# Optimization experiments

Measured on AMD Instinct MI355X. Metric: run time of the kernel, lower is better.

The kernel has to match this reference:

```python
import jax, jax.numpy as jnp
import numpy as np

DIM = 1024


def setup_inputs() -> dict:
    key = jax.random.key(0)
    ks = jax.random.split(key, 9)
    s = 1.0 / np.sqrt(DIM)
    x = jax.random.normal(ks[0], (4, 4096, DIM), dtype=jnp.float32)
    Wq = jax.random.uniform(ks[1], (DIM, DIM), jnp.float32, -s, s)
    bq = jax.random.uniform(ks[2], (DIM,), jnp.float32, -s, s)
    Wk = jax.random.uniform(ks[3], (DIM, DIM), jnp.float32, -s, s)
    bk = jax.random.uniform(ks[4], (DIM,), jnp.float32, -s, s)
    Wv = jax.random.uniform(ks[5], (DIM, DIM), jnp.float32, -s, s)
    bv = jax.random.uniform(ks[6], (DIM,), jnp.float32, -s, s)
    Wo = jax.random.uniform(ks[7], (DIM, DIM), jnp.float32, -s, s)
    bo = jax.random.uniform(ks[8], (DIM,), jnp.float32, -s, s)
    return {"x": x, "Wq": Wq, "bq": bq, "Wk": Wk, "bk": bk,
            "Wv": Wv, "bv": bv, "Wo": Wo, "bo": bo}


def reference(x, Wq, bq, Wk, bk, Wv, bv, Wo, bo):
    # x: [B, N, C]; weights stored as [C, C] (torch Linear applies x @ W.T,
    # here we store W already transposed so x @ W matches).
    scale = x.shape[-1] ** (-0.5)
    q = x @ Wq + bq                                  # [B, N, C]
    k = x @ Wk + bk
    v = x @ Wv + bv
    scores = jnp.einsum('bnc,bmc->bnm', q, k) * scale  # [B, N, N]
    attn = jax.nn.softmax(scores, axis=-1)
    out = jnp.einsum('bnm,bmc->bnc', attn, v)          # [B, N, C]
    return out @ Wo + bo
```

## Files before the change

### kernel.cpp

```cpp
#include <hip/hip_runtime.h>
#include <hip/hip_bf16.h>
#include <stdint.h>

typedef __bf16 bf16_8 __attribute__((ext_vector_type(8)));
typedef float  f32x4  __attribute__((ext_vector_type(4)));

#define GLL(g, l) __builtin_amdgcn_global_load_lds(                         \
    (__attribute__((address_space(1))) void*)(g),                           \
    (__attribute__((address_space(3))) void*)(l), 16, 0, 0)

__global__ void sniff_dtype(const uint32_t* __restrict__ x, uint32_t* __restrict__ flag)
{
    uint32_t w = x[threadIdx.x];
    uint32_t e = (w >> 23) & 0xFF;
    int isf32 = (e >= 100 && e <= 145) ? 1 : 0;
    unsigned long long m = __ballot(isf32);
    if (threadIdx.x == 0) *flag = (__popcll(m) >= 48) ? 1u : 0u;
}

__global__ __launch_bounds__(256)
void convert_to_bf16(const void* __restrict__ in, long elemOff,
                     __bf16* __restrict__ out, long n, const uint32_t* __restrict__ flag)
{
    long i = ((long)blockIdx.x * 256 + threadIdx.x) * 8;
    if (i >= n) return;
    bf16_8 o;
    if (*flag) {
        const float* p = (const float*)in + elemOff + i;
        float4 a = *(const float4*)p;
        float4 b = *(const float4*)(p + 4);
        o[0]=(__bf16)a.x; o[1]=(__bf16)a.y; o[2]=(__bf16)a.z; o[3]=(__bf16)a.w;
        o[4]=(__bf16)b.x; o[5]=(__bf16)b.y; o[6]=(__bf16)b.z; o[7]=(__bf16)b.w;
    } else {
        o = *(const bf16_8*)((const __bf16*)in + elemOff + i);
    }
    *(bf16_8*)(out + i) = o;
}

__global__ __launch_bounds__(256)
void convert_bias4(const void* b0, const void* b1, const void* b2, const void* b3,
                   __bf16* o0, __bf16* o1, __bf16* o2, __bf16* o3,
                   const uint32_t* __restrict__ flag)
{
    const void* in = (blockIdx.x == 0) ? b0 : (blockIdx.x == 1) ? b1
                   : (blockIdx.x == 2) ? b2 : b3;
    __bf16* out = (blockIdx.x == 0) ? o0 : (blockIdx.x == 1) ? o1
                : (blockIdx.x == 2) ? o2 : o3;
    long i = (long)threadIdx.x * 8;
    if (i >= 1024) return;
    bf16_8 o;
    if (*flag) {
        const float* p = (const float*)in + i;
        float4 a = *(const float4*)p;
        float4 b = *(const float4*)(p + 4);
        o[0]=(__bf16)a.x; o[1]=(__bf16)a.y; o[2]=(__bf16)a.z; o[3]=(__bf16)a.w;
        o[4]=(__bf16)b.x; o[5]=(__bf16)b.y; o[6]=(__bf16)b.z; o[7]=(__bf16)b.w;
    } else {
        o = *(const bf16_8*)((const __bf16*)in + i);
    }
    *(bf16_8*)(out + i) = o;
}

__global__ __launch_bounds__(256)
void convT_w4(const void* W0, const void* W1, const void* W2, const void* W3,
              __bf16* T0, __bf16* T1, __bf16* T2, __bf16* T3,
              const uint32_t* __restrict__ flag)
{
    const void* W = (blockIdx.z == 0) ? W0 : (blockIdx.z == 1) ? W1
                  : (blockIdx.z == 2) ? W2 : W3;
    __bf16* WT    = (blockIdx.z == 0) ? T0 : (blockIdx.z == 1) ? T1
                  : (blockIdx.z == 2) ? T2 : T3;
    __shared__ __bf16 tile[64][72];
    const int bc = blockIdx.x * 64, br = blockIdx.y * 64;
    const int c = threadIdx.x & 63, r0 = threadIdx.x >> 6;
    const bool f32 = (*flag != 0);
#pragma unroll
    for (int i = 0; i < 16; i++) {
        int r = i * 4 + r0;
        long idx = (long)(br + r) * 1024 + bc + c;
        float v = f32 ? ((const float*)W)[idx] : (float)((const __bf16*)W)[idx];
        tile[r][c] = (__bf16)v;
    }
    __syncthreads();
#pragma unroll
    for (int i = 0; i < 16; i++) {
        int r = i * 4 + r0;
        WT[(long)(bc + r) * 1024 + br + c] = tile[c][r];
    }
}

template<int BM_T, int BN_T, int GX, int GY, int GZ, int RX, int RY,
         int OUT_MODE, bool HAS_BIAS>
__global__ __launch_bounds__(512, 2)
void gemm_big(const __bf16* __restrict__ A, int lda,
              const __bf16* __restrict__ BT, int ldb,
              void* __restrict__ C, int ldc,
              const __bf16* __restrict__ bias,
              int kLen, long zCbytes, float scale,
              float* __restrict__ rowSums)
{
    constexpr int MT  = BM_T / 32;
    constexpr int NT  = BN_T / 64;
    constexpr int AG  = BM_T / 128;
    constexpr int BG  = BN_T / 128;
    constexpr int NLD = 2 * (AG + BG);

    constexpr int NRX = GX / RX;
    static_assert(NRX * ((GY * GZ) / RY) == 8, "regions must cover 8 XCDs");
    static_assert(RX * RY == (GX * GY * GZ) / 8, "region size = blocks/XCD");

    __shared__ __align__(16) __bf16 As[2][2 * BM_T * 32];
    __shared__ __align__(16) __bf16 Bs[2][2 * BN_T * 32];

    const int t    = threadIdx.x;
    const int wave = t >> 6;
    const int lane = t & 63;
    const int quad = lane >> 4;
    const int lrow = lane & 15;
    const int wm   = wave >> 2;
    const int wn   = wave & 3;

    const int h   = (int)blockIdx.x;
    const int xcd = h & 7;
    const int s   = h >> 3;
    const int bx  = (xcd % NRX) * RX + (s % RX);
    const int byz = (xcd / NRX) * RY + (s / RX);
    const int by  = byz % GY;
    const int bz  = byz / GY;

    const long m0  = (long)by * BM_T;
    const long n0  = (long)bx * BN_T;

    A  += (long)bz * kLen;
    BT += (long)bz * kLen;
    C   = (void*)((char*)C + (long)bz * zCbytes);

    const int sr = lane >> 2;
    const int sc = (lane & 3) ^ ((lane >> 3) & 3);
    const int sl = (lrow >> 1) & 3;

    const __bf16* aSrc = A + (m0 + wave * (BM_T / 8) + sr) * (long)lda + sc * 8;
    const __bf16* bSrc = BT + (n0 + wave * (BN_T / 8) + sr) * (long)ldb + sc * 8;

    f32x4 zero4 = {0.f, 0.f, 0.f, 0.f};
    f32x4 acc[MT][NT];
#pragma unroll
    for (int mt = 0; mt < MT; mt++)
#pragma unroll
        for (int nt = 0; nt < NT; nt++) acc[mt][nt] = zero4;

    auto STAGE = [&](int buf, const __bf16* aS, const __bf16* bS) {
        __bf16* aD = &As[buf][0] + wave * (BM_T / 8) * 32;
        __bf16* bD = &Bs[buf][0] + wave * (BN_T / 8) * 32;
#pragma unroll
        for (int kk = 0; kk < 2; kk++) {
#pragma unroll
            for (int g = 0; g < AG; g++)
                GLL(aS + kk * 32 + (long)g * 16 * lda,
                    aD + kk * (BM_T * 32) + g * 512);
#pragma unroll
            for (int g = 0; g < BG; g++)
                GLL(bS + kk * 32 + (long)g * 16 * ldb,
                    bD + kk * (BN_T * 32) + g * 512);
        }
    };

    auto COMPUTE = [&](int buf) {
#pragma unroll
        for (int kk = 0; kk < 2; kk++) {
            bf16_8 af[MT], bfr[NT];
#pragma unroll
            for (int mt = 0; mt < MT; mt++)
                af[mt] = *(const bf16_8*)(&As[buf][0] + kk * (BM_T * 32)
                           + (wm * (BM_T / 2) + mt * 16 + lrow) * 32 + (quad ^ sl) * 8);
#pragma unroll
            for (int nt = 0; nt < NT; nt++)
                bfr[nt] = *(const bf16_8*)(&Bs[buf][0] + kk * (BN_T * 32)
                           + (wn * (BN_T / 4) + nt * 16 + lrow) * 32 + (quad ^ sl) * 8);

#pragma unroll
            for (int mt = 0; mt < MT; mt++)
#pragma unroll
                for (int nt = 0; nt < NT; nt++)
                    acc[mt][nt] = __builtin_amdgcn_mfma_f32_16x16x32_bf16(
                                      af[mt], bfr[nt], acc[mt][nt], 0, 0, 0);
        }
    };

    STAGE(0, aSrc, bSrc);
    aSrc += 64; bSrc += 64;

    int cur = 0;
    for (int k0 = 64; k0 < kLen; k0 += 64) {
        STAGE(cur ^ 1, aSrc, bSrc);
        aSrc += 64; bSrc += 64;
        if constexpr (NLD == 8) asm volatile("s_waitcnt vmcnt(8)" ::: "memory");
        else                    asm volatile("s_waitcnt vmcnt(6)" ::: "memory");
        __builtin_amdgcn_s_barrier();
        __builtin_amdgcn_sched_barrier(0);
        __builtin_amdgcn_s_setprio(1);
        COMPUTE(cur);
        __builtin_amdgcn_s_setprio(0);
        asm volatile("s_waitcnt lgkmcnt(0)" ::: "memory");
        __builtin_amdgcn_s_barrier();
        __builtin_amdgcn_sched_barrier(0);
        cur ^= 1;
    }
    asm volatile("s_waitcnt vmcnt(0)" ::: "memory");
    __builtin_amdgcn_s_barrier();
    __builtin_amdgcn_sched_barrier(0);
    __builtin_amdgcn_s_setprio(1);
    COMPUTE(cur);
    __builtin_amdgcn_s_setprio(0);

    if (OUT_MODE == 3) {
#pragma unroll
        for (int mt = 0; mt < MT; mt++) {
#pragma unroll
            for (int i = 0; i < 4; i++) {
                long row = m0 + wm * (BM_T / 2) + mt * 16 + quad * 4 + i;
                float rs = 0.f;
#pragma unroll
                for (int nt = 0; nt < NT; nt++) {
                    long col = n0 + wn * (BN_T / 4) + nt * 16 + lrow;
                    float e = exp2f(acc[mt][nt][i] * scale);
                    ((__bf16*)C)[row * (long)ldc + col] = (__bf16)e;
                    rs += e;
                }
                rs += __shfl_xor(rs, 1);
                rs += __shfl_xor(rs, 2);
                rs += __shfl_xor(rs, 4);
                rs += __shfl_xor(rs, 8);
                if (lrow == 0) atomicAdd(&rowSums[row], rs);
            }
        }
        return;
    }

#pragma unroll
    for (int mt = 0; mt < MT; mt++) {
#pragma unroll
        for (int nt = 0; nt < NT; nt++) {
#pragma unroll
            for (int i = 0; i < 4; i++) {
                long row = m0 + wm * (BM_T / 2) + mt * 16 + quad * 4 + i;
                long col = n0 + wn * (BN_T / 4) + nt * 16 + lrow;
                float v = acc[mt][nt][i] * scale;
                if (HAS_BIAS) v += (float)bias[col];
                if (OUT_MODE == 0)      ((__bf16*)C)[row * (long)ldc + col] = (__bf16)v;
                else if (OUT_MODE == 1) ((__bf16*)C)[col * (long)ldc + row] = (__bf16)v;
                else                    ((float* )C)[row * (long)ldc + col] = v;
            }
        }
    }
}

template<int BN_T, int OUT_MODE, bool HAS_BIAS>
__global__ __launch_bounds__(256)
void gemm_bt(const __bf16* __restrict__ A, int lda,
             const __bf16* __restrict__ BT, int ldb,
             void* __restrict__ C, int ldc,
             const __bf16* __restrict__ bias,
             int M, int N, int kLen, long zCbytes, float scale,
             float* __restrict__ rowSums)
{
    constexpr int NT    = (BN_T == 128) ? 4 : 2;
    constexpr int BHALF = BN_T * 32;
    __shared__ __align__(16) __bf16 As[2][2 * 128 * 32];
    __shared__ __align__(16) __bf16 Bs[2][2 * BHALF];

    const int t    = threadIdx.x;
    const int wave = t >> 6;
    const int lane = t & 63;
    const int quad = lane >> 4;
    const int lrow = lane & 15;
    const int wm   = wave >> 1;
    const int wn   = wave & 1;
    const long m0  = (long)blockIdx.y * 128;
    const long n0  = (long)blockIdx.x * BN_T;

    A  += (long)blockIdx.z * kLen;
    BT += (long)blockIdx.z * kLen;
    C   = (void*)((char*)C + (long)blockIdx.z * zCbytes);

    const int sr = lane >> 2;
    const int sc = (lane & 3) ^ ((lane >> 3) & 3);

    const __bf16* aSrc = A + (m0 + wave * 32 + sr) * (long)lda + sc * 8;
    const __bf16* bSrc = (BN_T == 128)
        ? BT + (n0 + wave * 32 + sr) * (long)ldb + sc * 8
        : BT + (n0 + wave * 16 + sr) * (long)ldb + sc * 8;
    const long a16 = 16L * lda, b16 = 16L * ldb;

    f32x4 zero4 = {0.f, 0.f, 0.f, 0.f};
    f32x4 acc[4][NT];
#pragma unroll
    for (int mt = 0; mt < 4; mt++)
#pragma unroll
        for (int nt = 0; nt < NT; nt++) acc[mt][nt] = zero4;

    const int sl = (lrow >> 1) & 3;

    auto STAGE = [&](int buf, const __bf16* aS, const __bf16* bS) {
        __bf16* aD = &As[buf][0] + wave * 1024;
        __bf16* bD = &Bs[buf][0] + wave * (BN_T == 128 ? 1024 : 512);
        GLL(aS, aD);
        GLL(aS + a16, aD + 512);
        GLL(bS, bD);
        if (BN_T == 128) GLL(bS + b16, bD + 512);
        GLL(aS + 32, aD + 4096);
        GLL(aS + a16 + 32, aD + 4096 + 512);
        GLL(bS + 32, bD + BHALF);
        if (BN_T == 128) GLL(bS + b16 + 32, bD + BHALF + 512);
    };

    auto COMPUTE = [&](int buf) {
#pragma unroll
        for (int kk = 0; kk < 2; kk++) {
            bf16_8 af[4], bfr[NT];
#pragma unroll
            for (int mt = 0; mt < 4; mt++)
                af[mt] = *(const bf16_8*)(&As[buf][0] + kk * 4096
                           + (wm * 64 + mt * 16 + lrow) * 32 + (quad ^ sl) * 8);
#pragma unroll
            for (int nt = 0; nt < NT; nt++)
                bfr[nt] = *(const bf16_8*)(&Bs[buf][0] + kk * BHALF
                           + (wn * (BN_T / 2) + nt * 16 + lrow) * 32 + (quad ^ sl) * 8);

#pragma unroll
            for (int mt = 0; mt < 4; mt++)
#pragma unroll
                for (int nt = 0; nt < NT; nt++)
                    acc[mt][nt] = __builtin_amdgcn_mfma_f32_16x16x32_bf16(
                                      af[mt], bfr[nt], acc[mt][nt], 0, 0, 0);
        }
    };

    STAGE(0, aSrc, bSrc);
    aSrc += 64; bSrc += 64;
    __syncthreads();

    int cur = 0;
    for (int k0 = 64; k0 < kLen; k0 += 64) {
        STAGE(cur ^ 1, aSrc, bSrc);
        aSrc += 64; bSrc += 64;
        COMPUTE(cur);
        __syncthreads();
        cur ^= 1;
    }
    COMPUTE(cur);

    if (OUT_MODE == 3) {
#pragma unroll
        for (int mt = 0; mt < 4; mt++) {
#pragma unroll
            for (int i = 0; i < 4; i++) {
                long row = m0 + wm * 64 + mt * 16 + quad * 4 + i;
                float rs = 0.f;
#pragma unroll
                for (int nt = 0; nt < NT; nt++) {
                    long col = n0 + wn * (BN_T / 2) + nt * 16 + lrow;
                    float e = exp2f(acc[mt][nt][i] * scale);
                    ((__bf16*)C)[row * (long)ldc + col] = (__bf16)e;
                    rs += e;
                }
                rs += __shfl_xor(rs, 1);
                rs += __shfl_xor(rs, 2);
                rs += __shfl_xor(rs, 4);
                rs += __shfl_xor(rs, 8);
                if (lrow == 0) atomicAdd(&rowSums[row], rs);
            }
        }
        return;
    }

#pragma unroll
    for (int mt = 0; mt < 4; mt++) {
#pragma unroll
        for (int nt = 0; nt < NT; nt++) {
#pragma unroll
            for (int i = 0; i < 4; i++) {
                long row = m0 + wm * 64 + mt * 16 + quad * 4 + i;
                long col = n0 + wn * (BN_T / 2) + nt * 16 + lrow;
                float v = acc[mt][nt][i] * scale;
                if (HAS_BIAS) v += (float)bias[col];
                if (OUT_MODE == 0)      ((__bf16*)C)[row * (long)ldc + col] = (__bf16)v;
                else if (OUT_MODE == 1) ((__bf16*)C)[col * (long)ldc + row] = (__bf16)v;
                else                    ((float* )C)[row * (long)ldc + col] = v;
            }
        }
    }
}

__global__ __launch_bounds__(256)
void softmax_f32_to_bf16(float* __restrict__ S)
{
    float* srow = S + (long)blockIdx.x * 4096;
    __bf16* prow = (__bf16*)srow;
    const int t  = threadIdx.x;
    const int wv = t >> 6, ln = t & 63;

    float4 vv[4];
    float m = -1e30f;
#pragma unroll
    for (int i = 0; i < 4; i++) {
        vv[i] = ((const float4*)srow)[t + i * 256];
        m = fmaxf(m, fmaxf(fmaxf(vv[i].x, vv[i].y), fmaxf(vv[i].z, vv[i].w)));
    }
#pragma unroll
    for (int o = 32; o; o >>= 1) m = fmaxf(m, __shfl_xor(m, o));
    __shared__ float redm[4];
    if (ln == 0) redm[wv] = m;
    __syncthreads();
    m = fmaxf(fmaxf(redm[0], redm[1]), fmaxf(redm[2], redm[3]));

    const float L2E = 1.4426950408889634f;
    float s = 0.f;
#pragma unroll
    for (int i = 0; i < 4; i++) {
        vv[i].x = exp2f((vv[i].x - m) * L2E);
        vv[i].y = exp2f((vv[i].y - m) * L2E);
        vv[i].z = exp2f((vv[i].z - m) * L2E);
        vv[i].w = exp2f((vv[i].w - m) * L2E);
        s += vv[i].x + vv[i].y + vv[i].z + vv[i].w;
    }
#pragma unroll
    for (int o = 32; o; o >>= 1) s += __shfl_xor(s, o);
    __shared__ float reds[4];
    if (ln == 0) reds[wv] = s;
    __syncthreads();
    s = reds[0] + reds[1] + reds[2] + reds[3];
    float inv = 1.f / s;

    __syncthreads();
#pragma unroll
    for (int i = 0; i < 4; i++) {
        long base = (long)(t + i * 256) * 4;
        prow[base + 0] = (__bf16)(vv[i].x * inv);
        prow[base + 1] = (__bf16)(vv[i].y * inv);
        prow[base + 2] = (__bf16)(vv[i].z * inv);
        prow[base + 3] = (__bf16)(vv[i].w * inv);
    }
}

__global__ __launch_bounds__(256)
void reduce2_to_bf16(const float* __restrict__ Sf, __bf16* __restrict__ ao)
{
    const long i = blockIdx.x;
    const float* p = Sf + 4096 * i + 2048;
    const int t = threadIdx.x;
    float4 a = ((const float4*)p)[t];
    float4 b = ((const float4*)(p + 1024))[t];
    __bf16* o = ao + i * 1024 + t * 4;
    o[0] = (__bf16)(a.x + b.x);
    o[1] = (__bf16)(a.y + b.y);
    o[2] = (__bf16)(a.z + b.z);
    o[3] = (__bf16)(a.w + b.w);
}

__global__ __launch_bounds__(256)
void reduce2_scaled(const float* __restrict__ part, const float* __restrict__ sums,
                    __bf16* __restrict__ ao)
{
    const long i = blockIdx.x;
    const float inv = 1.0f / sums[i];
    const float* p = part + i * 2048;
    const int t = threadIdx.x;
    float4 a = ((const float4*)p)[t];
    float4 b = ((const float4*)(p + 1024))[t];
    __bf16* o = ao + i * 1024 + t * 4;
    o[0] = (__bf16)((a.x + b.x) * inv);
    o[1] = (__bf16)((a.y + b.y) * inv);
    o[2] = (__bf16)((a.z + b.z) * inv);
    o[3] = (__bf16)((a.w + b.w) * inv);
}

__global__ void fill_const_f32(float* p, long n, float val)
{
    long i = (long)blockIdx.x * 256 + threadIdx.x;
    if (i < n) p[i] = val;
}

extern "C" void kernel_launch(void* const* d_in, const int* in_sizes, int n_in,
                              void* d_out, int out_size, void* d_ws, size_t ws_size,
                              hipStream_t stream)
{
    const void* x  = d_in[0];
    const void* Wq = d_in[1];
    const void* bq = d_in[2];
    const void* Wk = d_in[3];
    const void* bk = d_in[4];
    const void* Wv = d_in[5];
    const void* bv = d_in[6];
    const void* Wo = d_in[7];
    const void* bo = d_in[8];

    const int  Bb = 4, Nn = 4096, Cc = 1024;
    const long seqB = (long)Nn * Cc;
    const long allR = (long)Bb * Nn;

    auto pad = [](size_t b) { return (b + 255) & ~(size_t)255; };
    const size_t szW    = (size_t)Cc * Cc * 2;
    const size_t szBias = (size_t)Cc * 2;
    const size_t szSeq  = (size_t)seqB * 2;
    const size_t szAll  = (size_t)allR * Cc * 2;

    const size_t fixed = pad(256) + 4 * pad(szW) + 4 * pad(szBias) + pad(szAll);
    const size_t needB = fixed + 4 * pad(szSeq);
    const size_t needA = fixed + 4 * pad(szAll);

    dim3 blk(256);
    dim3 blk5(512);

    if (ws_size < needB) {
        float val = 3000.0f + (float)(ws_size >> 20);
        fill_const_f32<<<dim3((out_size + 255) / 256), blk, 0, stream>>>(
            (float*)d_out, out_size, val);
        return;
    }

    const bool batched = (ws_size >= needA);

    char* ws = (char*)d_ws;
    size_t off = 0;
    auto alloc = [&](size_t bytes) -> char* { char* p = ws + off; off += pad(bytes); return p; };

    uint32_t* flag = (uint32_t*)alloc(256);
    __bf16* WqT = (__bf16*)alloc(szW);
    __bf16* WkT = (__bf16*)alloc(szW);
    __bf16* WvT = (__bf16*)alloc(szW);
    __bf16* WoT = (__bf16*)alloc(szW);
    __bf16* bqc = (__bf16*)alloc(szBias);
    __bf16* bkc = (__bf16*)alloc(szBias);
    __bf16* bvc = (__bf16*)alloc(szBias);
    __bf16* boc = (__bf16*)alloc(szBias);
    __bf16* ao  = (__bf16*)alloc(szAll);
    const size_t tierSz = batched ? szAll : szSeq;
    __bf16* xc  = (__bf16*)alloc(tierSz);
    __bf16* q   = (__bf16*)alloc(tierSz);
    __bf16* k   = (__bf16*)alloc(tierSz);
    __bf16* vT  = (__bf16*)alloc(tierSz);

    sniff_dtype<<<dim3(1), dim3(64), 0, stream>>>((const uint32_t*)x, flag);
    convT_w4<<<dim3(16, 16, 4), blk, 0, stream>>>(Wq, Wk, Wv, Wo, WqT, WkT, WvT, WoT, flag);
    convert_bias4<<<dim3(4), blk, 0, stream>>>(bq, bk, bv, bo, bqc, bkc, bvc, boc, flag);

    const float scale    = 0.03125f;
    const float scaleL2E = 0.03125f * 1.4426950408889634f;

    if (batched) {
        convert_to_bf16<<<dim3(allR * Cc / 2048), blk, 0, stream>>>(x, 0, xc, allR * Cc, flag);

        gemm_big<256, 256, 4, 64, 1, 4, 8, 0, true><<<dim3(256), blk5, 0, stream>>>(
            xc, Cc, WqT, Cc, q,  Cc,  bqc, Cc, 0, 1.f, nullptr);
        gemm_big<256, 256, 4, 64, 1, 4, 8, 0, true><<<dim3(256), blk5, 0, stream>>>(
            xc, Cc, WkT, Cc, k,  Cc,  bkc, Cc, 0, 1.f, nullptr);
        gemm_big<256, 256, 4, 64, 1, 4, 8, 1, true><<<dim3(256), blk5, 0, stream>>>(
            xc, Cc, WvT, Cc, vT, (int)allR, bvc, Cc, 0, 1.f, nullptr);

        float* sums4 = (float*)xc;
        fill_const_f32<<<dim3(64), blk, 0, stream>>>(sums4, 4L * Nn, 0.f);

        __bf16* P   = (__bf16*)d_out;
        float* part = (float*)((char*)d_out + (size_t)Nn * Nn * 2);

        for (int b = 0; b < Bb; b++) {
            const __bf16* qb  = q + (long)b * seqB;
            const __bf16* kb  = k + (long)b * seqB;
            const __bf16* vTb = vT + (long)b * Nn;
            float* sums = sums4 + (long)b * Nn;

            gemm_big<256, 256, 16, 16, 1, 8, 4, 3, false><<<dim3(256), blk5, 0, stream>>>(
                qb, Cc, kb, Cc, P, Nn, nullptr, Cc, 0, scaleL2E, sums);

            gemm_big<256, 128, 8, 16, 2, 8, 4, 2, false><<<dim3(256), blk5, 0, stream>>>(
                P, Nn, vTb, (int)allR, part, 2048,
                nullptr, Nn / 2, 4096 , 1.f, nullptr);

            reduce2_scaled<<<dim3(Nn), blk, 0, stream>>>(
                part, sums, ao + (long)b * seqB);
        }

        gemm_big<256, 256, 4, 64, 1, 4, 8, 2, true><<<dim3(256), blk5, 0, stream>>>(
            ao, Cc, WoT, Cc, (float*)d_out, Cc, boc, Cc, 0, 1.f, nullptr);
    } else {
        float* S = (float*)d_out;
        for (int b = 0; b < Bb; b++) {
            convert_to_bf16<<<dim3(seqB / 2048), blk, 0, stream>>>(x, b * seqB, xc, seqB, flag);
            dim3 gProj(Cc / 64, Nn / 128);
            gemm_bt<64, 0, true><<<gProj, blk, 0, stream>>>(xc, Cc, WqT, Cc, q,  Cc, bqc, Nn, Cc, Cc, 0, 1.f, nullptr);
            gemm_bt<64, 0, true><<<gProj, blk, 0, stream>>>(xc, Cc, WkT, Cc, k,  Cc, bkc, Nn, Cc, Cc, 0, 1.f, nullptr);
            gemm_bt<64, 1, true><<<gProj, blk, 0, stream>>>(xc, Cc, WvT, Cc, vT, Nn, bvc, Nn, Cc, Cc, 0, 1.f, nullptr);

            gemm_bt<128, 2, false><<<dim3(Nn / 128, Nn / 128), blk, 0, stream>>>(
                q, Cc, k, Cc, S, Nn, nullptr, Nn, Nn, Cc, 0, scale, nullptr);

            softmax_f32_to_bf16<<<dim3(Nn), blk, 0, stream>>>(S);

            gemm_bt<128, 2, false><<<dim3(Cc / 128, Nn / 128, 2), blk, 0, stream>>>(
                (const __bf16*)S, 2 * Nn, vT, Nn, (float*)S + 2048, Nn,
                nullptr, Nn, Cc, Nn / 2, 4096, 1.f, nullptr);

            reduce2_to_bf16<<<dim3(Nn), blk, 0, stream>>>(S, ao + (long)b * seqB);
        }

        gemm_bt<128, 2, true><<<dim3(Cc / 128, (int)(allR / 128)), blk, 0, stream>>>(
            ao, Cc, WoT, Cc, (float*)d_out, Cc, boc, (int)allR, Cc, Cc, 0, 1.f, nullptr);
    }
}
```

Before: 769.9 us.

## Restructure GEMM main loop into 4-slot K=32 ring with split-phase MFMA

Replaces the two-buffer, 64-deep K staging with a four-slot ring of 32-deep K slices prefetched three slices ahead. Each iteration is split into two half-M compute phases, with LDS fragment reads and the next slice's global loads interleaved between barriers. The aim is to hide global-load latency and spread LDS reads across MFMA work. It doubles the barriers per K step and hardcodes MT=8 (loops over 4 plus 4 rows), so it is only correct for BM_T=256 tiles.

```diff
diff --git a/kernel.cpp b/kernel.cpp
--- a/kernel.cpp
+++ b/kernel.cpp
@@ -103,14 +103,14 @@
     constexpr int NT  = BN_T / 64;
     constexpr int AG  = BM_T / 128;
     constexpr int BG  = BN_T / 128;
-    constexpr int NLD = 2 * (AG + BG);
+    constexpr int L   = AG + BG;
 
     constexpr int NRX = GX / RX;
     static_assert(NRX * ((GY * GZ) / RY) == 8, "regions must cover 8 XCDs");
     static_assert(RX * RY == (GX * GY * GZ) / 8, "region size = blocks/XCD");
 
-    __shared__ __align__(16) __bf16 As[2][2 * BM_T * 32];
-    __shared__ __align__(16) __bf16 Bs[2][2 * BN_T * 32];
+    __shared__ __align__(16) __bf16 As[4 * BM_T * 32];
+    __shared__ __align__(16) __bf16 Bs[4 * BN_T * 32];
 
     const int t    = threadIdx.x;
     const int wave = t >> 6;
@@ -122,9 +122,9 @@
 
     const int h   = (int)blockIdx.x;
     const int xcd = h & 7;
-    const int s   = h >> 3;
-    const int bx  = (xcd % NRX) * RX + (s % RX);
-    const int byz = (xcd / NRX) * RY + (s / RX);
+    const int s0_ = h >> 3;
+    const int bx  = (xcd % NRX) * RX + (s0_ % RX);
+    const int byz = (xcd / NRX) * RY + (s0_ / RX);
     const int by  = byz % GY;
     const int bz  = byz / GY;
 
@@ -139,8 +139,8 @@
     const int sc = (lane & 3) ^ ((lane >> 3) & 3);
     const int sl = (lrow >> 1) & 3;
 
-    const __bf16* aSrc = A + (m0 + wave * (BM_T / 8) + sr) * (long)lda + sc * 8;
-    const __bf16* bSrc = BT + (n0 + wave * (BN_T / 8) + sr) * (long)ldb + sc * 8;
+    const __bf16* aStage = A + (m0 + wave * (BM_T / 8) + sr) * (long)lda + sc * 8;
+    const __bf16* bStage = BT + (n0 + wave * (BN_T / 8) + sr) * (long)ldb + sc * 8;
 
     f32x4 zero4 = {0.f, 0.f, 0.f, 0.f};
     f32x4 acc[MT][NT];
@@ -149,69 +149,89 @@
 #pragma unroll
         for (int nt = 0; nt < NT; nt++) acc[mt][nt] = zero4;
 
-    auto STAGE = [&](int buf, const __bf16* aS, const __bf16* bS) {
-        __bf16* aD = &As[buf][0] + wave * (BM_T / 8) * 32;
-        __bf16* bD = &Bs[buf][0] + wave * (BN_T / 8) * 32;
-#pragma unroll
-        for (int kk = 0; kk < 2; kk++) {
-#pragma unroll
-            for (int g = 0; g < AG; g++)
-                GLL(aS + kk * 32 + (long)g * 16 * lda,
-                    aD + kk * (BM_T * 32) + g * 512);
-#pragma unroll
-            for (int g = 0; g < BG; g++)
-                GLL(bS + kk * 32 + (long)g * 16 * ldb,
-                    bD + kk * (BN_T * 32) + g * 512);
-        }
+    auto STAGE_SLICE = [&](int slice) {
+        const int slot = slice & 3;
+        __bf16* aD = As + slot * (BM_T * 32) + wave * (BM_T / 8) * 32;
+        __bf16* bD = Bs + slot * (BN_T * 32) + wave * (BN_T / 8) * 32;
+#pragma unroll
+        for (int g = 0; g < AG; g++)
+            GLL(aStage + (long)g * 16 * lda, aD + g * 512);
+#pragma unroll
+        for (int g = 0; g < BG; g++)
+            GLL(bStage + (long)g * 16 * ldb, bD + g * 512);
+        aStage += 32; bStage += 32;
     };
 
-    auto COMPUTE = [&](int buf) {
-#pragma unroll
-        for (int kk = 0; kk < 2; kk++) {
-            bf16_8 af[MT], bfr[NT];
-#pragma unroll
-            for (int mt = 0; mt < MT; mt++)
-                af[mt] = *(const bf16_8*)(&As[buf][0] + kk * (BM_T * 32)
-                           + (wm * (BM_T / 2) + mt * 16 + lrow) * 32 + (quad ^ sl) * 8);
+    const int S = kLen >> 5;
+
+    STAGE_SLICE(0);
+    STAGE_SLICE(1);
+    STAGE_SLICE(2);
+    if constexpr (L == 4) asm volatile("s_waitcnt vmcnt(8)" ::: "memory");
+    else                  asm volatile("s_waitcnt vmcnt(6)" ::: "memory");
+    __builtin_amdgcn_s_barrier();
+    __builtin_amdgcn_sched_barrier(0);
+
+    for (int s = 0; s < S; s++) {
+        const int slot = s & 3;
+        const __bf16* slotA = As + slot * (BM_T * 32);
+        const __bf16* slotB = Bs + slot * (BN_T * 32);
+
+        bf16_8 afA[4], bfr[NT];
+#pragma unroll
+        for (int mt = 0; mt < 4; mt++)
+            afA[mt] = *(const bf16_8*)(slotA
+                        + (wm * (BM_T / 2) + mt * 16 + lrow) * 32 + (quad ^ sl) * 8);
+#pragma unroll
+        for (int nt = 0; nt < NT; nt++)
+            bfr[nt] = *(const bf16_8*)(slotB
+                        + (wn * (BN_T / 4) + nt * 16 + lrow) * 32 + (quad ^ sl) * 8);
+        if (s + 3 < S) STAGE_SLICE(s + 3);
+
+        __builtin_amdgcn_s_barrier();
+        asm volatile("s_waitcnt lgkmcnt(0)" ::: "memory");
+        __builtin_amdgcn_sched_barrier(0);
+        __builtin_amdgcn_s_setprio(1);
+#pragma unroll
+        for (int mt = 0; mt < 4; mt++)
 #pragma unroll
             for (int nt = 0; nt < NT; nt++)
-                bfr[nt] = *(const bf16_8*)(&Bs[buf][0] + kk * (BN_T * 32)
-                           + (wn * (BN_T / 4) + nt * 16 + lrow) * 32 + (quad ^ sl) * 8);
-
-#pragma unroll
-            for (int mt = 0; mt < MT; mt++)
-#pragma unroll
-                for (int nt = 0; nt < NT; nt++)
-                    acc[mt][nt] = __builtin_amdgcn_mfma_f32_16x16x32_bf16(
-                                      af[mt], bfr[nt], acc[mt][nt], 0, 0, 0);
-        }
-    };
-
-    STAGE(0, aSrc, bSrc);
-    aSrc += 64; bSrc += 64;
-
-    int cur = 0;
-    for (int k0 = 64; k0 < kLen; k0 += 64) {
-        STAGE(cur ^ 1, aSrc, bSrc);
-        aSrc += 64; bSrc += 64;
-        if constexpr (NLD == 8) asm volatile("s_waitcnt vmcnt(8)" ::: "memory");
-        else                    asm volatile("s_waitcnt vmcnt(6)" ::: "memory");
+                acc[mt][nt] = __builtin_amdgcn_mfma_f32_16x16x32_bf16(
+                                  afA[mt], bfr[nt], acc[mt][nt], 0, 0, 0);
+        __builtin_amdgcn_s_setprio(0);
         __builtin_amdgcn_s_barrier();
         __builtin_amdgcn_sched_barrier(0);
+
+        bf16_8 afB[4];
+#pragma unroll
+        for (int mt = 0; mt < 4; mt++)
+            afB[mt] = *(const bf16_8*)(slotA
+                        + (wm * (BM_T / 2) + (mt + 4) * 16 + lrow) * 32 + (quad ^ sl) * 8);
+
+        if (s + 4 <= S) {
+            if constexpr (L == 4) asm volatile("s_waitcnt vmcnt(8)" ::: "memory");
+            else                  asm volatile("s_waitcnt vmcnt(6)" ::: "memory");
+        } else if (s + 3 == S) {
+            if constexpr (L == 4) asm volatile("s_waitcnt vmcnt(4)" ::: "memory");
+            else                  asm volatile("s_waitcnt vmcnt(3)" ::: "memory");
+        } else if (s + 2 == S) {
+            asm volatile("s_waitcnt vmcnt(0)" ::: "memory");
+        }
+
+        __builtin_amdgcn_s_barrier();
+        asm volatile("s_waitcnt lgkmcnt(0)" ::: "memory");
+        __builtin_amdgcn_sched_barrier(0);
         __builtin_amdgcn_s_setprio(1);
-        COMPUTE(cur);
+#pragma unroll
+        for (int mt = 0; mt < 4; mt++)
+#pragma unroll
+            for (int nt = 0; nt < NT; nt++)
+                acc[mt + 4][nt] = __builtin_amdgcn_mfma_f32_16x16x32_bf16(
+                                      afB[mt], bfr[nt], acc[mt + 4][nt], 0, 0, 0);
         __builtin_amdgcn_s_setprio(0);
-        asm volatile("s_waitcnt lgkmcnt(0)" ::: "memory");
         __builtin_amdgcn_s_barrier();
         __builtin_amdgcn_sched_barrier(0);
-        cur ^= 1;
-    }
-    asm volatile("s_waitcnt vmcnt(0)" ::: "memory");
-    __builtin_amdgcn_s_barrier();
-    __builtin_amdgcn_sched_barrier(0);
-    __builtin_amdgcn_s_setprio(1);
-    COMPUTE(cur);
-    __builtin_amdgcn_s_setprio(0);
+    }
 
     if (OUT_MODE == 3) {
 #pragma unroll
```

Measured after the change: 768.2 us. Within noise of the previous version (-0.2%).
